# Kernel tuning notes

Hardware: AMD Instinct MI355X
Metric: run time of the kernel (lower is better)

## Reference

```python
import jax, jax.numpy as jnp
import numpy as np


def setup_inputs() -> dict:
    key = jax.random.key(0)
    k1, k2 = jax.random.split(key)
    B, L, C, H, W = 1, 16, 8, 128, 128
    # flows scaled so cumulative displacements stay mostly inside [-1, 1]
    flows = jax.random.normal(k1, (B, L, 2, H, W), jnp.float32) * 0.1
    images = jax.random.normal(k2, (B, L, C, H, W), jnp.float32)
    return {"flows": flows, "images": images}


def _base_grid(H, W, dtype):
    step_y, step_x = 2.0 / H, 2.0 / W
    gy = jnp.linspace(-1.0 + step_y * 0.5, 1.0 - step_y * 0.5, H, dtype=dtype)
    gx = jnp.linspace(-1.0 + step_x * 0.5, 1.0 - step_x * 0.5, W, dtype=dtype)
    mx, my = jnp.meshgrid(gx, gy, indexing="xy")  # each [H, W]
    return jnp.stack([mx, my], axis=-1)  # [H, W, 2], (x, y)


def _grid_sample_bilinear(img, grid):
    # img: [C, H, W]; grid: [H, W, 2] normalized coords in [-1, 1]
    # matches torch grid_sample(mode='bilinear', padding_mode='zeros', align_corners=False)
    C, H, W = img.shape
    ix = (grid[..., 0] + 1.0) * (W * 0.5) - 0.5
    iy = (grid[..., 1] + 1.0) * (H * 0.5) - 0.5
    x0 = jnp.floor(ix)
    y0 = jnp.floor(iy)
    wx = ix - x0
    wy = iy - y0

    def gather(xf, yf):
        xi = xf.astype(jnp.int32)
        yi = yf.astype(jnp.int32)
        valid = ((xf >= 0) & (xf < W) & (yf >= 0) & (yf < H)).astype(img.dtype)
        xi = jnp.clip(xi, 0, W - 1)
        yi = jnp.clip(yi, 0, H - 1)
        return img[:, yi, xi] * valid  # [C, H, W]

    return (
        gather(x0, y0) * ((1.0 - wx) * (1.0 - wy))
        + gather(x0 + 1.0, y0) * (wx * (1.0 - wy))
        + gather(x0, y0 + 1.0) * ((1.0 - wx) * wy)
        + gather(x0 + 1.0, y0 + 1.0) * (wx * wy)
    )


def reference(flows, images):
    B, L, C, H, W = images.shape
    dtype = flows.dtype
    cum = jnp.cumsum(flows.astype(jnp.float32), axis=1).astype(dtype)  # [B,L,2,H,W]
    base = _base_grid(H, W, dtype)  # [H,W,2]

    # pairwise relative flow: rel[b,t,k] = cum[b,t] - cum[b,k]  -> [B,L,L,2,H,W]
    rel = cum[:, :, None] - cum[:, None, :]
    grid = base + jnp.transpose(rel, (0, 1, 2, 4, 5, 3))  # [B,L,L,H,W,2]
    gx = jnp.remainder(grid[..., 0] + 1.0, 2.0) - 1.0  # wrap x periodically
    grid = jnp.concatenate([gx[..., None], grid[..., 1:]], axis=-1)

    # sample images[b,k] at grid[b,t,k]
    sample_k = jax.vmap(_grid_sample_bilinear, in_axes=(0, 0))       # over k
    sample_tk = jax.vmap(sample_k, in_axes=(None, 0))                # over t
    sample_btk = jax.vmap(sample_tk, in_axes=(0, 0))                 # over b
    sampled = sample_btk(images, grid)  # [B,L,L,C,H,W]

    # triangular accumulation: out[b,t] = sum_{k<=t} sampled[b,t,k]
    mask = jnp.tril(jnp.ones((L, L), dtype=dtype))
    return jnp.einsum("btkchw,tk->btchw", sampled, mask)
```

## Files before the change

### kernel.cpp

```cpp
#include <hip/hip_runtime.h>
#include <hip/hip_fp16.h>

constexpr int L = 16, C = 8, H = 128, W = 128;
constexpr int HW = H * W;
constexpr int CHW = C * HW;

__global__ __launch_bounds__(256) void prep_k(const float* __restrict__ flows,
                                              const float* __restrict__ images,
                                              float* __restrict__ cum,
                                              __half* __restrict__ timg) {
    int b = blockIdx.x;
    constexpr int TB = (L * HW) / 256;
    if (b < TB) {
        int idx = b * 256 + threadIdx.x;
        int l = idx >> 14, pix = idx & (HW - 1);
        const float* src = images + (size_t)l * CHW + pix;
        float v0 = __builtin_nontemporal_load(src + 0 * HW);
        float v1 = __builtin_nontemporal_load(src + 1 * HW);
        float v2 = __builtin_nontemporal_load(src + 2 * HW);
        float v3 = __builtin_nontemporal_load(src + 3 * HW);
        float v4 = __builtin_nontemporal_load(src + 4 * HW);
        float v5 = __builtin_nontemporal_load(src + 5 * HW);
        float v6 = __builtin_nontemporal_load(src + 6 * HW);
        float v7 = __builtin_nontemporal_load(src + 7 * HW);
        float4 packed;
        __half2* hp = reinterpret_cast<__half2*>(&packed);
        hp[0] = __floats2half2_rn(v0, v1);
        hp[1] = __floats2half2_rn(v2, v3);
        hp[2] = __floats2half2_rn(v4, v5);
        hp[3] = __floats2half2_rn(v6, v7);
        reinterpret_cast<float4*>(timg)[idx] = packed;
    } else {
        int idx = (b - TB) * 256 + threadIdx.x;
        int comp = idx >> 14, pix = idx & (HW - 1);
        const float* src = flows + comp * HW + pix;
        float* dst = cum + comp * HW + pix;
        float s = 0.f;
#pragma unroll
        for (int l = 0; l < L; ++l) {
            s += __builtin_nontemporal_load(src + (size_t)l * 2 * HW);
            dst[(size_t)l * 2 * HW] = s;
        }
    }
}

__device__ __forceinline__ void samp(float acc[8], float relx, float rely,
                                     float bx1, float by1,
                                     const __half* __restrict__ img) {
    float xr = bx1 + relx;
    xr = fmaf(-2.0f, floorf(xr * 0.5f), xr);
    float yr = by1 + rely;
    float ix = fmaf(xr, W * 0.5f, -0.5f);
    float iy = fmaf(yr, H * 0.5f, -0.5f);
    float x0f = floorf(ix), y0f = floorf(iy);
    float wx = ix - x0f, wy = iy - y0f;
    int x0 = (int)x0f, y0 = (int)y0f;

    float wx0 = ((unsigned)x0       < (unsigned)W) ? 1.f - wx : 0.f;
    float wx1 = ((unsigned)(x0 + 1) < (unsigned)W) ? wx       : 0.f;
    float wy0 = ((unsigned)y0       < (unsigned)H) ? 1.f - wy : 0.f;
    float wy1 = ((unsigned)(y0 + 1) < (unsigned)H) ? wy       : 0.f;
    int xi0 = min(max(x0, 0), W - 1), xi1 = min(max(x0 + 1, 0), W - 1);
    int yi0 = min(max(y0, 0), H - 1), yi1 = min(max(y0 + 1, 0), H - 1);

    const float4* p = reinterpret_cast<const float4*>(img);
    float4 r00 = p[yi0 * W + xi0];
    float4 r01 = p[yi0 * W + xi1];
    float4 r10 = p[yi1 * W + xi0];
    float4 r11 = p[yi1 * W + xi1];
    float w00 = wx0 * wy0, w01 = wx1 * wy0, w10 = wx0 * wy1, w11 = wx1 * wy1;
    const __half* h00 = reinterpret_cast<const __half*>(&r00);
    const __half* h01 = reinterpret_cast<const __half*>(&r01);
    const __half* h10 = reinterpret_cast<const __half*>(&r10);
    const __half* h11 = reinterpret_cast<const __half*>(&r11);
#pragma unroll
    for (int c = 0; c < 8; ++c) {
        float v = fmaf(__half2float(h00[c]), w00,
                  fmaf(__half2float(h01[c]), w01,
                  fmaf(__half2float(h10[c]), w10,
                       __half2float(h11[c]) * w11)));
        acc[c] += v;
    }
}

constexpr int TPB = 256;
__global__ __launch_bounds__(TPB) void sample_k(const float* __restrict__ cum,
                                                const __half* __restrict__ timg,
                                                float* __restrict__ out) {
    int p   = blockIdx.x >> 6;
    int pix = (blockIdx.x & 63) * TPB + threadIdx.x;
    int h = pix >> 7, w = pix & (W - 1);
    float bx1 = (w + 0.5f) * (2.0f / W);
    float by1 = (h + 0.5f) * (2.0f / H);

    int t1 = p, t2 = 15 - p;
    float c1x = cum[(size_t)(2 * t1)     * HW + pix];
    float c1y = cum[(size_t)(2 * t1 + 1) * HW + pix];
    float c2x = cum[(size_t)(2 * t2)     * HW + pix];
    float c2y = cum[(size_t)(2 * t2 + 1) * HW + pix];

    float acc1[8] = {0, 0, 0, 0, 0, 0, 0, 0};
    float acc2[8] = {0, 0, 0, 0, 0, 0, 0, 0};

    for (int k = 0; k <= t2; ++k) {
        float ckx = cum[(size_t)(2 * k)     * HW + pix];
        float cky = cum[(size_t)(2 * k + 1) * HW + pix];
        const __half* img = timg + (size_t)k * HW * C;
        samp(acc2, c2x - ckx, c2y - cky, bx1, by1, img);
        if (k <= t1)
            samp(acc1, c1x - ckx, c1y - cky, bx1, by1, img);
    }

    size_t o1 = (size_t)t1 * CHW + pix;
    size_t o2 = (size_t)t2 * CHW + pix;
#pragma unroll
    for (int c = 0; c < 8; ++c) {
        __builtin_nontemporal_store(acc1[c], out + o1 + (size_t)c * HW);
        __builtin_nontemporal_store(acc2[c], out + o2 + (size_t)c * HW);
    }
}

extern "C" void kernel_launch(void* const* d_in, const int* in_sizes, int n_in,
                              void* d_out, int out_size, void* d_ws, size_t ws_size,
                              hipStream_t stream) {
    const float* flows  = (const float*)d_in[0];
    const float* images = (const float*)d_in[1];
    float* out = (float*)d_out;

    float*  cum  = (float*)d_ws;
    __half* timg = (__half*)((char*)d_ws + (size_t)2 * L * HW * 4);

    prep_k<<<(L * HW) / 256 + (2 * HW) / 256, 256, 0, stream>>>(flows, images, cum, timg);
    sample_k<<<8 * (HW / TPB), TPB, 0, stream>>>(cum, timg, out);
}
```

Measured before the change: 88.57 us.

## Fuse flow cumsum into sampler and use 2D 16x8 pixel tiles

Removes the cumulative-flow computation from the prep kernel. Each sampling thread now builds its own prefix sums from the raw flows in registers, which drops the cum workspace round trip and its per-k global loads. The sampler also switches to 128-thread blocks covering 16x8 2D tiles, so neighbouring bilinear taps share cache lines. Nontemporal loads and stores become plain accesses. The cost is redundant cumsum work across the 8 pair-blocks and more register pressure from the 32 prefix values, which dynamic indexing may spill to scratch.

```diff
diff --git a/kernel.cpp b/kernel.cpp
--- a/kernel.cpp
+++ b/kernel.cpp
@@ -5,43 +5,18 @@
 constexpr int HW = H * W;
 constexpr int CHW = C * HW;
 
-__global__ __launch_bounds__(256) void prep_k(const float* __restrict__ flows,
-                                              const float* __restrict__ images,
-                                              float* __restrict__ cum,
+__global__ __launch_bounds__(256) void prep_k(const float* __restrict__ images,
                                               __half* __restrict__ timg) {
-    int b = blockIdx.x;
-    constexpr int TB = (L * HW) / 256;
-    if (b < TB) {
-        int idx = b * 256 + threadIdx.x;
-        int l = idx >> 14, pix = idx & (HW - 1);
-        const float* src = images + (size_t)l * CHW + pix;
-        float v0 = __builtin_nontemporal_load(src + 0 * HW);
-        float v1 = __builtin_nontemporal_load(src + 1 * HW);
-        float v2 = __builtin_nontemporal_load(src + 2 * HW);
-        float v3 = __builtin_nontemporal_load(src + 3 * HW);
-        float v4 = __builtin_nontemporal_load(src + 4 * HW);
-        float v5 = __builtin_nontemporal_load(src + 5 * HW);
-        float v6 = __builtin_nontemporal_load(src + 6 * HW);
-        float v7 = __builtin_nontemporal_load(src + 7 * HW);
-        float4 packed;
-        __half2* hp = reinterpret_cast<__half2*>(&packed);
-        hp[0] = __floats2half2_rn(v0, v1);
-        hp[1] = __floats2half2_rn(v2, v3);
-        hp[2] = __floats2half2_rn(v4, v5);
-        hp[3] = __floats2half2_rn(v6, v7);
-        reinterpret_cast<float4*>(timg)[idx] = packed;
-    } else {
-        int idx = (b - TB) * 256 + threadIdx.x;
-        int comp = idx >> 14, pix = idx & (HW - 1);
-        const float* src = flows + comp * HW + pix;
-        float* dst = cum + comp * HW + pix;
-        float s = 0.f;
-#pragma unroll
-        for (int l = 0; l < L; ++l) {
-            s += __builtin_nontemporal_load(src + (size_t)l * 2 * HW);
-            dst[(size_t)l * 2 * HW] = s;
-        }
-    }
+    int idx = blockIdx.x * 256 + threadIdx.x;
+    int l = idx >> 14, pix = idx & (HW - 1);
+    const float* src = images + (size_t)l * CHW + pix;
+    float4 packed;
+    __half2* hp = reinterpret_cast<__half2*>(&packed);
+    hp[0] = __floats2half2_rn(src[0 * HW], src[1 * HW]);
+    hp[1] = __floats2half2_rn(src[2 * HW], src[3 * HW]);
+    hp[2] = __floats2half2_rn(src[4 * HW], src[5 * HW]);
+    hp[3] = __floats2half2_rn(src[6 * HW], src[7 * HW]);
+    reinterpret_cast<float4*>(timg)[idx] = packed;
 }
 
 __device__ __forceinline__ void samp(float acc[8], float relx, float rely,
@@ -83,40 +58,52 @@
     }
 }
 
-constexpr int TPB = 256;
-__global__ __launch_bounds__(TPB) void sample_k(const float* __restrict__ cum,
+constexpr int TPB = 128;
+__global__ __launch_bounds__(TPB) void sample_k(const float* __restrict__ flows,
                                                 const __half* __restrict__ timg,
                                                 float* __restrict__ out) {
-    int p   = blockIdx.x >> 6;
-    int pix = (blockIdx.x & 63) * TPB + threadIdx.x;
-    int h = pix >> 7, w = pix & (W - 1);
+    int b    = blockIdx.x;
+    int p    = b >> 7;
+    int tile = b & 127;
+    int Tx = tile & 7, Ty = tile >> 3;
+    int tx = threadIdx.x & 15, ty = threadIdx.x >> 4;
+    int w = Tx * 16 + tx, h = Ty * 8 + ty;
+    int pix = h * W + w;
+
     float bx1 = (w + 0.5f) * (2.0f / W);
     float by1 = (h + 0.5f) * (2.0f / H);
 
+    float Px[L], Py[L];
+    {
+        float sx = 0.f, sy = 0.f;
+#pragma unroll
+        for (int j = 0; j < L; ++j) {
+            sx += flows[(size_t)(2 * j)     * HW + pix];
+            sy += flows[(size_t)(2 * j + 1) * HW + pix];
+            Px[j] = sx; Py[j] = sy;
+        }
+    }
+
     int t1 = p, t2 = 15 - p;
-    float c1x = cum[(size_t)(2 * t1)     * HW + pix];
-    float c1y = cum[(size_t)(2 * t1 + 1) * HW + pix];
-    float c2x = cum[(size_t)(2 * t2)     * HW + pix];
-    float c2y = cum[(size_t)(2 * t2 + 1) * HW + pix];
+    float c1x = Px[t1], c1y = Py[t1];
+    float c2x = Px[t2], c2y = Py[t2];
 
     float acc1[8] = {0, 0, 0, 0, 0, 0, 0, 0};
     float acc2[8] = {0, 0, 0, 0, 0, 0, 0, 0};
 
     for (int k = 0; k <= t2; ++k) {
-        float ckx = cum[(size_t)(2 * k)     * HW + pix];
-        float cky = cum[(size_t)(2 * k + 1) * HW + pix];
         const __half* img = timg + (size_t)k * HW * C;
-        samp(acc2, c2x - ckx, c2y - cky, bx1, by1, img);
+        samp(acc2, c2x - Px[k], c2y - Py[k], bx1, by1, img);
         if (k <= t1)
-            samp(acc1, c1x - ckx, c1y - cky, bx1, by1, img);
+            samp(acc1, c1x - Px[k], c1y - Py[k], bx1, by1, img);
     }
 
     size_t o1 = (size_t)t1 * CHW + pix;
     size_t o2 = (size_t)t2 * CHW + pix;
 #pragma unroll
     for (int c = 0; c < 8; ++c) {
-        __builtin_nontemporal_store(acc1[c], out + o1 + (size_t)c * HW);
-        __builtin_nontemporal_store(acc2[c], out + o2 + (size_t)c * HW);
+        out[o1 + (size_t)c * HW] = acc1[c];
+        out[o2 + (size_t)c * HW] = acc2[c];
     }
 }
 
@@ -127,9 +114,8 @@
     const float* images = (const float*)d_in[1];
     float* out = (float*)d_out;
 
-    float*  cum  = (float*)d_ws;
-    __half* timg = (__half*)((char*)d_ws + (size_t)2 * L * HW * 4);
+    __half* timg = (__half*)d_ws;
 
-    prep_k<<<(L * HW) / 256 + (2 * HW) / 256, 256, 0, stream>>>(flows, images, cum, timg);
-    sample_k<<<8 * (HW / TPB), TPB, 0, stream>>>(cum, timg, out);
+    prep_k<<<(L * HW) / 256, 256, 0, stream>>>(images, timg);
+    sample_k<<<8 * 128, TPB, 0, stream>>>(flows, timg, out);
 }
```

Measured after the change: 85.48 us, median of 2. -3.5%, faster.
